# Kernel tuning notes

Measured on AMD Instinct MI355X. Metric: run time of the kernel, lower is better.

The kernel has to match this reference:

```python
import jax, jax.numpy as jnp
import numpy as np

N_ITERATIONS = 3
EPS = 1e-07


def squash(t, axis=-1):
    sqr_norm = jnp.sum(t * t, axis=axis, keepdims=True)
    norm = jnp.sqrt(sqr_norm + EPS)
    return sqr_norm * t / ((1.0 + sqr_norm) * norm)


def setup_inputs() -> dict:
    key = jax.random.key(0)
    B, N_IN, N_OUT, D = 256, 1152, 10, 16
    u_hat = jax.random.normal(key, (B, N_IN, N_OUT, D, 1), dtype=jnp.float32)
    return {"u_hat": u_hat}


def reference(u_hat):
    # u_hat: [B, n_in, n_out, d, 1]
    B, n_in, n_out = u_hat.shape[0], u_hat.shape[1], u_hat.shape[2]
    b = jnp.zeros((B, n_in, n_out, 1, 1), dtype=u_hat.dtype)
    v = None
    for r in range(N_ITERATIONS):
        c = jax.nn.softmax(b, axis=1)                      # softmax over input caps
        s = jnp.sum(c * u_hat, axis=1, keepdims=True)      # [B, 1, n_out, d, 1]
        v = squash(s, axis=-2)                             # squash over capsule dim
        if r < N_ITERATIONS - 1:
            # u_hat^T @ v (broadcast v over input caps): agreement [B, n_in, n_out, 1, 1]
            a = jnp.sum(u_hat * v, axis=-2, keepdims=True)
            b = b + a
    return jnp.squeeze(v, axis=1)                          # [B, n_out, d, 1]
```

## Files before the change

kernel.cpp:

```cpp
#include <hip/hip_runtime.h>

#define BATCH 256
#define NIN   1152
#define NOUT  10
#define DDIM  16
#define KPT   18

__global__ __launch_bounds__(256)
void routing_kernel(const float* __restrict__ u_hat, float* __restrict__ out) {
    __shared__ float bsh[NIN];
    __shared__ float wsh[NIN];
    __shared__ float red[4 * DDIM];
    __shared__ float vsh[DDIM];
    __shared__ float scal[8];

    const int t    = threadIdx.x;
    const int q    = t & 3;
    const int g    = t >> 2;
    const int wave = t >> 6;
    const int lane = t & 63;

    const int x   = blockIdx.x;
    const int xcd = x & 7;
    const int j   = x >> 3;
    const int oo  = j % NOUT;
    const int bb  = xcd * 32 + j / NOUT;

    const float* base = u_hat + (size_t)bb * (NIN * NOUT * DDIM) + oo * DDIM + q * 4;

    float4 u[KPT];
#pragma unroll
    for (int k = 0; k < KPT; ++k) {
        const int i = g + 64 * k;
        u[k] = *reinterpret_cast<const float4*>(base + (size_t)i * (NOUT * DDIM));
    }

    for (int i = t; i < NIN; i += 256) bsh[i] = 0.0f;
    __syncthreads();

    for (int r = 0; r < 3; ++r) {
        float m = -3.4e38f;
        for (int i = t; i < NIN; i += 256) m = fmaxf(m, bsh[i]);
        for (int off = 32; off >= 1; off >>= 1) m = fmaxf(m, __shfl_down(m, off));
        if (lane == 0) scal[wave] = m;
        __syncthreads();
        m = fmaxf(fmaxf(scal[0], scal[1]), fmaxf(scal[2], scal[3]));

        float z = 0.0f;
        for (int i = t; i < NIN; i += 256) {
            const float w = __expf(bsh[i] - m);
            wsh[i] = w;
            z += w;
        }
        for (int off = 32; off >= 1; off >>= 1) z += __shfl_down(z, off);
        if (lane == 0) scal[4 + wave] = z;
        __syncthreads();
        const float invZ = 1.0f / (scal[4] + scal[5] + scal[6] + scal[7]);

        float sx = 0.f, sy = 0.f, sz = 0.f, sw = 0.f;
#pragma unroll
        for (int k = 0; k < KPT; ++k) {
            const float w = wsh[g + 64 * k];
            sx += w * u[k].x; sy += w * u[k].y; sz += w * u[k].z; sw += w * u[k].w;
        }
        for (int off = 32; off >= 4; off >>= 1) {
            sx += __shfl_down(sx, off);
            sy += __shfl_down(sy, off);
            sz += __shfl_down(sz, off);
            sw += __shfl_down(sw, off);
        }
        if (lane < 4) {
            float* rp = &red[wave * DDIM + lane * 4];
            rp[0] = sx; rp[1] = sy; rp[2] = sz; rp[3] = sw;
        }
        __syncthreads();
        if (t < DDIM) {
            vsh[t] = (red[t] + red[DDIM + t] + red[2 * DDIM + t] + red[3 * DDIM + t]) * invZ;
        }
        __syncthreads();

        float sqr = 0.0f;
#pragma unroll
        for (int d = 0; d < DDIM; ++d) { const float sv = vsh[d]; sqr += sv * sv; }
        const float scale = sqr / ((1.0f + sqr) * sqrtf(sqr + 1e-7f));
        __syncthreads();
        if (t < DDIM) vsh[t] *= scale;
        __syncthreads();

        if (r == 2) break;

        const float vx = vsh[q * 4 + 0], vy = vsh[q * 4 + 1];
        const float vz = vsh[q * 4 + 2], vw = vsh[q * 4 + 3];
#pragma unroll
        for (int k = 0; k < KPT; ++k) {
            float a = u[k].x * vx + u[k].y * vy + u[k].z * vz + u[k].w * vw;
            a += __shfl_xor(a, 1);
            a += __shfl_xor(a, 2);
            if (q == 0) bsh[g + 64 * k] += a;
        }
        __syncthreads();
    }

    if (t < DDIM) {
        out[(size_t)(bb * NOUT + oo) * DDIM + t] = vsh[t];
    }
}

extern "C" void kernel_launch(void* const* d_in, const int* in_sizes, int n_in,
                              void* d_out, int out_size, void* d_ws, size_t ws_size,
                              hipStream_t stream) {
    const float* u_hat = (const float*)d_in[0];
    float* out = (float*)d_out;
    routing_kernel<<<dim3(BATCH * NOUT), dim3(256), 0, stream>>>(u_hat, out);
}
```

Measured before the change: 263.6 us.

## Use 512-thread blocks with half the register tile and fold squash scale

Doubles the block to 512 threads (8 waves), so each thread holds 9 float4 of u_hat in registers instead of 18, and the reductions grow to 8 partial slots. It also folds the squash scale into the v loads and the final store, which removes two barriers and a shared-memory write per iteration. The intent is more memory parallelism and latency hiding for the bandwidth-bound u_hat load. The cost is larger cross-wave reductions and heavier barriers per block.

Result: no change. 262.1 us (-0.6%).

```diff
diff --git a/kernel.cpp b/kernel.cpp
--- a/kernel.cpp
+++ b/kernel.cpp
@@ -4,15 +4,16 @@
 #define NIN   1152
 #define NOUT  10
 #define DDIM  16
-#define KPT   18
+#define KPT   9
 
-__global__ __launch_bounds__(256)
+__global__ __launch_bounds__(512, 6)
 void routing_kernel(const float* __restrict__ u_hat, float* __restrict__ out) {
     __shared__ float bsh[NIN];
     __shared__ float wsh[NIN];
-    __shared__ float red[4 * DDIM];
+    __shared__ float red[8][DDIM];
     __shared__ float vsh[DDIM];
-    __shared__ float scal[8];
+    __shared__ float smax[8];
+    __shared__ float ssum[8];
 
     const int t    = threadIdx.x;
     const int q    = t & 3;
@@ -31,36 +32,39 @@
     float4 u[KPT];
 #pragma unroll
     for (int k = 0; k < KPT; ++k) {
-        const int i = g + 64 * k;
+        const int i = g + 128 * k;
         u[k] = *reinterpret_cast<const float4*>(base + (size_t)i * (NOUT * DDIM));
     }
 
-    for (int i = t; i < NIN; i += 256) bsh[i] = 0.0f;
+    for (int i = t; i < NIN; i += 512) bsh[i] = 0.0f;
     __syncthreads();
 
+    float scale = 0.0f;
     for (int r = 0; r < 3; ++r) {
         float m = -3.4e38f;
-        for (int i = t; i < NIN; i += 256) m = fmaxf(m, bsh[i]);
+        for (int i = t; i < NIN; i += 512) m = fmaxf(m, bsh[i]);
         for (int off = 32; off >= 1; off >>= 1) m = fmaxf(m, __shfl_down(m, off));
-        if (lane == 0) scal[wave] = m;
+        if (lane == 0) smax[wave] = m;
         __syncthreads();
-        m = fmaxf(fmaxf(scal[0], scal[1]), fmaxf(scal[2], scal[3]));
+        m = fmaxf(fmaxf(fmaxf(smax[0], smax[1]), fmaxf(smax[2], smax[3])),
+                  fmaxf(fmaxf(smax[4], smax[5]), fmaxf(smax[6], smax[7])));
 
         float z = 0.0f;
-        for (int i = t; i < NIN; i += 256) {
+        for (int i = t; i < NIN; i += 512) {
             const float w = __expf(bsh[i] - m);
             wsh[i] = w;
             z += w;
         }
         for (int off = 32; off >= 1; off >>= 1) z += __shfl_down(z, off);
-        if (lane == 0) scal[4 + wave] = z;
+        if (lane == 0) ssum[wave] = z;
         __syncthreads();
-        const float invZ = 1.0f / (scal[4] + scal[5] + scal[6] + scal[7]);
+        const float invZ = 1.0f / (((ssum[0] + ssum[1]) + (ssum[2] + ssum[3])) +
+                                   ((ssum[4] + ssum[5]) + (ssum[6] + ssum[7])));
 
         float sx = 0.f, sy = 0.f, sz = 0.f, sw = 0.f;
 #pragma unroll
         for (int k = 0; k < KPT; ++k) {
-            const float w = wsh[g + 64 * k];
+            const float w = wsh[g + 128 * k];
             sx += w * u[k].x; sy += w * u[k].y; sz += w * u[k].z; sw += w * u[k].w;
         }
         for (int off = 32; off >= 4; off >>= 1) {
@@ -70,39 +74,37 @@
             sw += __shfl_down(sw, off);
         }
         if (lane < 4) {
-            float* rp = &red[wave * DDIM + lane * 4];
+            float* rp = &red[wave][lane * 4];
             rp[0] = sx; rp[1] = sy; rp[2] = sz; rp[3] = sw;
         }
         __syncthreads();
         if (t < DDIM) {
-            vsh[t] = (red[t] + red[DDIM + t] + red[2 * DDIM + t] + red[3 * DDIM + t]) * invZ;
+            vsh[t] = (((red[0][t] + red[1][t]) + (red[2][t] + red[3][t])) +
+                      ((red[4][t] + red[5][t]) + (red[6][t] + red[7][t]))) * invZ;
         }
         __syncthreads();
 
         float sqr = 0.0f;
 #pragma unroll
         for (int d = 0; d < DDIM; ++d) { const float sv = vsh[d]; sqr += sv * sv; }
-        const float scale = sqr / ((1.0f + sqr) * sqrtf(sqr + 1e-7f));
-        __syncthreads();
-        if (t < DDIM) vsh[t] *= scale;
-        __syncthreads();
+        scale = sqr / ((1.0f + sqr) * sqrtf(sqr + 1e-7f));
 
         if (r == 2) break;
 
-        const float vx = vsh[q * 4 + 0], vy = vsh[q * 4 + 1];
-        const float vz = vsh[q * 4 + 2], vw = vsh[q * 4 + 3];
+        const float vx = vsh[q * 4 + 0] * scale, vy = vsh[q * 4 + 1] * scale;
+        const float vz = vsh[q * 4 + 2] * scale, vw = vsh[q * 4 + 3] * scale;
 #pragma unroll
         for (int k = 0; k < KPT; ++k) {
             float a = u[k].x * vx + u[k].y * vy + u[k].z * vz + u[k].w * vw;
             a += __shfl_xor(a, 1);
             a += __shfl_xor(a, 2);
-            if (q == 0) bsh[g + 64 * k] += a;
+            if (q == 0) bsh[g + 128 * k] += a;
         }
         __syncthreads();
     }
 
     if (t < DDIM) {
-        out[(size_t)(bb * NOUT + oo) * DDIM + t] = vsh[t];
+        out[(size_t)(bb * NOUT + oo) * DDIM + t] = vsh[t] * scale;
     }
 }
 
@@ -111,5 +113,5 @@
                               hipStream_t stream) {
     const float* u_hat = (const float*)d_in[0];
     float* out = (float*)d_out;
-    routing_kernel<<<dim3(BATCH * NOUT), dim3(256), 0, stream>>>(u_hat, out);
+    routing_kernel<<<dim3(BATCH * NOUT), dim3(512), 0, stream>>>(u_hat, out);
 }
```
